# Optimization experiments

Measured on AMD Instinct MI355X. Metric: run time of the kernel, lower is better.

## Reference

```python
import jax, jax.numpy as jnp
import numpy as np

C = 2          # n_channels
F = 32         # n_fields
H = 1024       # hidden_size
B = 16         # batch
S = 2048       # sequence length


def setup_inputs() -> dict:
    key = jax.random.key(0)
    ks = jax.random.split(key, 5)
    hidden = jax.random.normal(ks[0], (B, S, H), dtype=jnp.float32)
    # per-channel learned parameters
    emb = jax.random.normal(ks[1], (C, F, H), dtype=jnp.float32) * 0.02
    scale = 1.0 / np.sqrt(H)
    Wk = jax.random.normal(ks[2], (C, H, H), dtype=jnp.float32) * scale
    Wq = jax.random.normal(ks[3], (C, H, H), dtype=jnp.float32) * scale
    Wv = jax.random.normal(ks[4], (C, H, H), dtype=jnp.float32) * scale
    return {"hidden": hidden, "emb": emb, "Wk": Wk, "Wq": Wq, "Wv": Wv}


def reference(hidden, emb, Wk, Wq, Wv):
    # per-channel linear projections (nn.Linear: x @ W.T), vectorized over channels
    # hidden: [B,S,H], W*: [C,H_out,H_in] -> [C,B,S,H]
    key = jnp.einsum('bsh,coh->cbso', hidden, Wk)
    query = jnp.einsum('bsh,coh->cbso', hidden, Wq)
    value = jnp.einsum('bsh,coh->cbso', hidden, Wv)
    # label embeddings broadcast across batch: [C,F,H] -> [C,B,F,H]
    lab = jnp.broadcast_to(emb[:, None, :, :], (C, hidden.shape[0], F, H))
    # concat label embeddings onto query along token axis: [C,B,S+F,H]
    query = jnp.concatenate([query, lab], axis=2)
    # attention scores (no softmax): [B,C,S+F,S]
    attention = jnp.einsum('cbih,cbjh->bcij', query, key)
    # score[b,c,j,i] = attention[b,c,j,i] * sum_h value[c,b,i,h]
    vsum = jnp.sum(value, axis=-1)          # [C,B,S]
    score = attention * jnp.transpose(vsum, (1, 0, 2))[:, :, None, :]
    return score
```

## Files before the change

kernel.cpp:

```cpp
#include <hip/hip_runtime.h>

typedef unsigned int u32;
typedef unsigned short ushort_t;

typedef __attribute__((ext_vector_type(4))) float f32x4;
typedef __attribute__((ext_vector_type(8))) __bf16 bf16x8;

#define Cc 2
#define Ff 32
#define Hh 1024
#define Bb 16
#define Ss 2048
#define SF 2080

__device__ __forceinline__ ushort_t f2bf(float f) {
  u32 u = __builtin_bit_cast(u32, f);
  u32 r = (u + 0x7fffu + ((u >> 16) & 1u)) >> 16;
  return (ushort_t)r;
}

typedef __attribute__((address_space(1))) const u32 u32_g;
typedef __attribute__((address_space(3))) u32 u32_l;

__device__ __forceinline__ void glds16(const void* g, void* l) {
  __builtin_amdgcn_global_load_lds((u32_g*)g, (u32_l*)l, 16, 0, 0);
}

__device__ __forceinline__ f32x4 mfma16(bf16x8 a, bf16x8 b, f32x4 c) {
  return __builtin_amdgcn_mfma_f32_16x16x32_bf16(a, b, c, 0, 0, 0);
}


__global__ void k_wvsum(const float* __restrict__ Wv, float* __restrict__ wvsum) {
  int idx = blockIdx.y * 256 + threadIdx.x;
  int c = idx >> 10, h = idx & 1023;
  int o0 = blockIdx.x * 128;
  const float* p = Wv + (size_t)c * Hh * Hh + (size_t)o0 * Hh + h;
  float s = 0.f;
#pragma unroll 4
  for (int o = 0; o < 128; ++o) s += p[(size_t)o * Hh];
  atomicAdd(&wvsum[c * Hh + h], s);
}

__global__ void k_hidden(const float* __restrict__ hidden, const float* __restrict__ wvsum,
                         ushort_t* __restrict__ hbf, float* __restrict__ vsum) {
  int row = blockIdx.x;
  int t = threadIdx.x;
  const float4 hv = reinterpret_cast<const float4*>(hidden + (size_t)row * Hh)[t];
  ushort4 o4;
  o4.x = f2bf(hv.x); o4.y = f2bf(hv.y); o4.z = f2bf(hv.z); o4.w = f2bf(hv.w);
  reinterpret_cast<ushort4*>(hbf + (size_t)row * Hh)[t] = o4;
  float4 w0 = reinterpret_cast<const float4*>(wvsum)[t];
  float4 w1 = reinterpret_cast<const float4*>(wvsum + Hh)[t];
  float d0 = hv.x * w0.x + hv.y * w0.y + hv.z * w0.z + hv.w * w0.w;
  float d1 = hv.x * w1.x + hv.y * w1.y + hv.z * w1.z + hv.w * w1.w;
  for (int off = 32; off > 0; off >>= 1) {
    d0 += __shfl_down(d0, off);
    d1 += __shfl_down(d1, off);
  }
  __shared__ float red[2][4];
  int wave = t >> 6, lane = t & 63;
  if (lane == 0) { red[0][wave] = d0; red[1][wave] = d1; }
  __syncthreads();
  if (t == 0) {
    vsum[row]            = red[0][0] + red[0][1] + red[0][2] + red[0][3];
    vsum[Bb * Ss + row]  = red[1][0] + red[1][1] + red[1][2] + red[1][3];
  }
}

__global__ void k_transpose(const float* __restrict__ Wk, const float* __restrict__ Wq,
                            ushort_t* __restrict__ WkT, ushort_t* __restrict__ WqT) {
  __shared__ float t[32][33];
  int zz = blockIdx.z; int mat = zz >> 1, c = zz & 1;
  const float* in = (mat ? Wq : Wk) + (size_t)c * Hh * Hh;
  ushort_t* out = (mat ? WqT : WkT) + (size_t)c * Hh * Hh;
  int h0 = blockIdx.x * 32, o0 = blockIdx.y * 32;
  int tx = threadIdx.x & 31, ty = threadIdx.x >> 5;
#pragma unroll
  for (int i = 0; i < 4; ++i)
    t[ty + 8 * i][tx] = in[(size_t)(o0 + ty + 8 * i) * Hh + h0 + tx];
  __syncthreads();
#pragma unroll
  for (int i = 0; i < 4; ++i)
    out[(size_t)(h0 + ty + 8 * i) * Hh + o0 + tx] = f2bf(t[tx][ty + 8 * i]);
}

__global__ void k_ef(const float* __restrict__ emb, const float* __restrict__ Wk,
                     float* __restrict__ ef) {
  int c = blockIdx.z;
  int h = blockIdx.y * 256 + threadIdx.x;
  int o0 = blockIdx.x * 128;
  __shared__ float es[Ff][129];
  for (int i = threadIdx.x; i < Ff * 128; i += 256) {
    int f = i >> 7, oo = i & 127;
    es[f][oo] = emb[(size_t)(c * Ff + f) * Hh + o0 + oo];
  }
  __syncthreads();
  float acc[Ff];
#pragma unroll
  for (int f = 0; f < Ff; ++f) acc[f] = 0.f;
  for (int oo = 0; oo < 128; ++oo) {
    float wk = Wk[(size_t)c * Hh * Hh + (size_t)(o0 + oo) * Hh + h];
#pragma unroll
    for (int f = 0; f < Ff; ++f) acc[f] += es[f][oo] * wk;
  }
#pragma unroll
  for (int f = 0; f < Ff; ++f)
    atomicAdd(&ef[(size_t)(c * Ff + f) * Hh + h], acc[f]);
}

__global__ void k_ef2g(const float* __restrict__ ef, ushort_t* __restrict__ Gaug) {
  int i = blockIdx.x * 256 + threadIdx.x;
  int c = i >> 15, f = (i >> 10) & 31, h = i & 1023;
  ushort_t v = f2bf(ef[i]);
#pragma unroll
  for (int b = 0; b < Bb; ++b)
    Gaug[((size_t)(c * Bb + b) * SF + Ss + f) * Hh + h] = v;
}

template <int MODE>
__global__ __launch_bounds__(256, 2) void gemm_nt(
    const ushort_t* __restrict__ Aall, const ushort_t* __restrict__ Ball,
    void* __restrict__ Oall, const float* __restrict__ scaleAll) {
  constexpr int BK = 64;
  const int tid = threadIdx.x;
  const int wave = tid >> 6, lane = tid & 63;
  const int wm = wave >> 1, wn = wave & 1;
  const int z = blockIdx.z;
  const int row0 = blockIdx.y * 128;
  const int col0 = blockIdx.x * 128;

  const ushort_t* A; const ushort_t* B;
  if constexpr (MODE == 0) {
    A = Aall + (size_t)z * Hh * Hh;
    B = Ball + (size_t)z * Hh * Hh;
  } else if constexpr (MODE == 1) {
    A = Aall;
    B = Ball + (size_t)z * Hh * Hh;
  } else {
    const int b = z & 15;
    A = Aall + (size_t)z * SF * Hh;
    B = Ball + (size_t)b * Ss * Hh;
  }

  __shared__ ushort_t As[128 * BK];
  __shared__ ushort_t Bs[128 * BK];

  const ushort_t* gA[4]; const ushort_t* gB[4];
  char* lA[4]; char* lB[4];
#pragma unroll
  for (int r = 0; r < 4; ++r) {
    int chunk = r * 256 + wave * 64 + lane;
    int rrow = chunk >> 3, kc = chunk & 7;
    gA[r] = A + (size_t)(row0 + rrow) * Hh + kc * 8;
    gB[r] = B + (size_t)(col0 + rrow) * Hh + kc * 8;
    lA[r] = (char*)As + (r * 256 + wave * 64) * 16;
    lB[r] = (char*)Bs + (r * 256 + wave * 64) * 16;
  }

  f32x4 acc[4][4];
#pragma unroll
  for (int i = 0; i < 4; ++i)
#pragma unroll
    for (int j = 0; j < 4; ++j) acc[i][j] = (f32x4){0.f, 0.f, 0.f, 0.f};

  const int lr = lane & 15, lk = lane >> 4;

  for (int kit = 0; kit < Hh / BK; ++kit) {
#pragma unroll
    for (int r = 0; r < 4; ++r) glds16(gA[r], lA[r]);
#pragma unroll
    for (int r = 0; r < 4; ++r) glds16(gB[r], lB[r]);
#pragma unroll
    for (int r = 0; r < 4; ++r) { gA[r] += BK; gB[r] += BK; }
    __syncthreads();
#pragma unroll
    for (int ks = 0; ks < 2; ++ks) {
      bf16x8 af[4], bfr[4];
#pragma unroll
      for (int mt = 0; mt < 4; ++mt)
        af[mt] = *reinterpret_cast<const bf16x8*>(
            (const char*)As + (wm * 64 + mt * 16 + lr) * 128 + ks * 64 + lk * 16);
#pragma unroll
      for (int nt = 0; nt < 4; ++nt)
        bfr[nt] = *reinterpret_cast<const bf16x8*>(
            (const char*)Bs + (wn * 64 + nt * 16 + lr) * 128 + ks * 64 + lk * 16);
#pragma unroll
      for (int mt = 0; mt < 4; ++mt)
#pragma unroll
        for (int nt = 0; nt < 4; ++nt)
          acc[mt][nt] = mfma16(af[mt], bfr[nt], acc[mt][nt]);
    }
    __syncthreads();
  }

  if constexpr (MODE == 2) {
    const int c = z >> 4, b = z & 15;
    float* Out = (float*)Oall + (size_t)(b * Cc + c) * SF * Ss;
    const float* scale = scaleAll + (size_t)c * (Bb * Ss) + (size_t)b * Ss;
#pragma unroll
    for (int nt = 0; nt < 4; ++nt) {
      int col = col0 + wn * 64 + nt * 16 + lr;
      float s = scale[col];
#pragma unroll
      for (int mt = 0; mt < 4; ++mt) {
        int rbase = row0 + wm * 64 + mt * 16 + lk * 4;
#pragma unroll
        for (int r = 0; r < 4; ++r) {
          int orow = rbase + r;
          if (orow < SF) Out[(size_t)orow * Ss + col] = acc[mt][nt][r] * s;
        }
      }
    }
  } else {
    ushort_t* Out;
    if constexpr (MODE == 0) Out = (ushort_t*)Oall + (size_t)z * Hh * Hh;
    else Out = (ushort_t*)Oall + (size_t)z * (Bb * SF * Hh);
#pragma unroll
    for (int nt = 0; nt < 4; ++nt) {
      int col = col0 + wn * 64 + nt * 16 + lr;
#pragma unroll
      for (int mt = 0; mt < 4; ++mt) {
        int rbase = row0 + wm * 64 + mt * 16 + lk * 4;
#pragma unroll
        for (int r = 0; r < 4; ++r) {
          int m = rbase + r;
          size_t orow;
          if constexpr (MODE == 1) orow = (size_t)(m >> 11) * SF + (m & 2047);
          else orow = (size_t)m;
          Out[orow * Hh + col] = f2bf(acc[mt][nt][r]);
        }
      }
    }
  }
}

extern "C" void kernel_launch(void* const* d_in, const int* in_sizes, int n_in,
                              void* d_out, int out_size, void* d_ws, size_t ws_size,
                              hipStream_t stream) {
  const float* hidden = (const float*)d_in[0];
  const float* emb    = (const float*)d_in[1];
  const float* Wk     = (const float*)d_in[2];
  const float* Wq     = (const float*)d_in[3];
  const float* Wv     = (const float*)d_in[4];
  float* out = (float*)d_out;

  char* base = (char*)d_ws;
  ushort_t* hbf   = (ushort_t*)(base);
  ushort_t* Gaug  = (ushort_t*)(base + 67108864);
  ushort_t* MTb   = (ushort_t*)(base + 203685888);
  ushort_t* WkT   = (ushort_t*)(base + 207880192);
  ushort_t* WqT   = (ushort_t*)(base + 212074496);
  float*    wvsum = (float*)  (base + 216268800);
  float*    efb   = (float*)  (base + 216276992);
  float*    vsum  = (float*)  (base + 216539136);

  hipMemsetAsync(wvsum, 0, 8192 + 262144, stream);

  k_wvsum<<<dim3(8, 8), 256, 0, stream>>>(Wv, wvsum);
  k_hidden<<<Bb * Ss, 256, 0, stream>>>(hidden, wvsum, hbf, vsum);
  k_transpose<<<dim3(32, 32, 4), 256, 0, stream>>>(Wk, Wq, WkT, WqT);
  k_ef<<<dim3(8, 4, 2), 256, 0, stream>>>(emb, Wk, efb);

  gemm_nt<0><<<dim3(8, 8, 2), 256, 0, stream>>>(WkT, WqT, MTb, nullptr);
  gemm_nt<1><<<dim3(8, 256, 2), 256, 0, stream>>>(hbf, MTb, Gaug, nullptr);
  k_ef2g<<<256, 256, 0, stream>>>(efb, Gaug);
  gemm_nt<2><<<dim3(16, 17, 32), 256, 0, stream>>>(Gaug, hbf, out, vsum);
}
```

Measured before the change: 1.324 ms.

## Double-buffer LDS tiles in gemm_nt and swizzle workgroup order across XCDs

Double-buffers the shared-memory A/B tiles so the global-to-LDS load for the next K step is issued before computing the current one. This leaves one barrier per iteration and lets memory latency overlap with MFMA work. It also remaps the flat workgroup id so that consecutive blocks are grouped by (fid mod 8), intended to keep tiles that share data on the same XCD's L2. The cost is doubled LDS use (64KB per block), which may limit occupancy at launch bounds of 2 blocks, and the remap hardcodes grid sizes per mode.

After: 1.477 ms. 11.5% more time.

```diff
diff --git a/kernel.cpp b/kernel.cpp
--- a/kernel.cpp
+++ b/kernel.cpp
@@ -123,12 +123,25 @@
     const ushort_t* __restrict__ Aall, const ushort_t* __restrict__ Ball,
     void* __restrict__ Oall, const float* __restrict__ scaleAll) {
   constexpr int BK = 64;
+  constexpr int NK = Hh / BK;
+  constexpr int GX = (MODE == 0) ? 8 : (MODE == 1) ? 8 : 16;
+  constexpr int GY = (MODE == 0) ? 8 : (MODE == 1) ? 256 : 17;
+  constexpr int GZ = (MODE == 0) ? 2 : (MODE == 1) ? 2 : 32;
+  constexpr int NWG = GX * GY * GZ;
+
   const int tid = threadIdx.x;
   const int wave = tid >> 6, lane = tid & 63;
   const int wm = wave >> 1, wn = wave & 1;
-  const int z = blockIdx.z;
-  const int row0 = blockIdx.y * 128;
-  const int col0 = blockIdx.x * 128;
+
+  int fid = blockIdx.x + GX * (blockIdx.y + GY * blockIdx.z);
+  int swz = (fid & 7) * (NWG >> 3) + (fid >> 3);
+  const int bx = swz % GX;
+  int tt = swz / GX;
+  const int by = tt % GY;
+  const int z  = tt / GY;
+
+  const int row0 = by * 128;
+  const int col0 = bx * 128;
 
   const ushort_t* A; const ushort_t* B;
   if constexpr (MODE == 0) {
@@ -143,8 +156,9 @@
     B = Ball + (size_t)b * Ss * Hh;
   }
 
-  __shared__ ushort_t As[128 * BK];
-  __shared__ ushort_t Bs[128 * BK];
+  __shared__ ushort_t As[2][128 * BK];
+  __shared__ ushort_t Bs[2][128 * BK];
+  constexpr int BUFB = 128 * BK * 2;
 
   const ushort_t* gA[4]; const ushort_t* gB[4];
   char* lA[4]; char* lB[4];
@@ -154,8 +168,8 @@
     int rrow = chunk >> 3, kc = chunk & 7;
     gA[r] = A + (size_t)(row0 + rrow) * Hh + kc * 8;
     gB[r] = B + (size_t)(col0 + rrow) * Hh + kc * 8;
-    lA[r] = (char*)As + (r * 256 + wave * 64) * 16;
-    lB[r] = (char*)Bs + (r * 256 + wave * 64) * 16;
+    lA[r] = (char*)&As[0][0] + (r * 256 + wave * 64) * 16;
+    lB[r] = (char*)&Bs[0][0] + (r * 256 + wave * 64) * 16;
   }
 
   f32x4 acc[4][4];
@@ -166,33 +180,47 @@
 
   const int lr = lane & 15, lk = lane >> 4;
 
-  for (int kit = 0; kit < Hh / BK; ++kit) {
-#pragma unroll
-    for (int r = 0; r < 4; ++r) glds16(gA[r], lA[r]);
-#pragma unroll
-    for (int r = 0; r < 4; ++r) glds16(gB[r], lB[r]);
+  auto stage = [&](int buf) {
+    const int boff = buf * BUFB;
+#pragma unroll
+    for (int r = 0; r < 4; ++r) glds16(gA[r], lA[r] + boff);
+#pragma unroll
+    for (int r = 0; r < 4; ++r) glds16(gB[r], lB[r] + boff);
 #pragma unroll
     for (int r = 0; r < 4; ++r) { gA[r] += BK; gB[r] += BK; }
-    __syncthreads();
+  };
+
+  auto compute = [&](int buf) {
+    const char* asb = (const char*)&As[buf][0];
+    const char* bsb = (const char*)&Bs[buf][0];
 #pragma unroll
     for (int ks = 0; ks < 2; ++ks) {
       bf16x8 af[4], bfr[4];
 #pragma unroll
       for (int mt = 0; mt < 4; ++mt)
         af[mt] = *reinterpret_cast<const bf16x8*>(
-            (const char*)As + (wm * 64 + mt * 16 + lr) * 128 + ks * 64 + lk * 16);
+            asb + (wm * 64 + mt * 16 + lr) * 128 + ks * 64 + lk * 16);
 #pragma unroll
       for (int nt = 0; nt < 4; ++nt)
         bfr[nt] = *reinterpret_cast<const bf16x8*>(
-            (const char*)Bs + (wn * 64 + nt * 16 + lr) * 128 + ks * 64 + lk * 16);
+            bsb + (wn * 64 + nt * 16 + lr) * 128 + ks * 64 + lk * 16);
 #pragma unroll
       for (int mt = 0; mt < 4; ++mt)
 #pragma unroll
         for (int nt = 0; nt < 4; ++nt)
           acc[mt][nt] = mfma16(af[mt], bfr[nt], acc[mt][nt]);
     }
+  };
+
+  stage(0);
+  __syncthreads();
+  for (int kit = 0; kit < NK - 1; ++kit) {
+    const int cur = kit & 1;
+    stage(cur ^ 1);
+    compute(cur);
     __syncthreads();
   }
+  compute((NK - 1) & 1);
 
   if constexpr (MODE == 2) {
     const int c = z >> 4, b = z & 15;
```

## Replace GEMM with 256x256-tile, 512-thread, multi-stage pipelined kernel

Applied to the files above, without the earlier changes.

Replaces the 128x128, single-buffered bf16 MFMA GEMM with 256x256 output tiles computed by 8 waves. Tiles are staged through a ring of LDS slots with BK=32 and loads issued three k-steps ahead, using explicit vmcnt/lgkmcnt waits and a single barrier per step. LDS reads use an XOR swizzle, MFMA sections get raised wave priority, and block IDs are remapped so neighbouring tiles land on the same XCD. The goal is more reuse per tile and global loads hidden behind MFMA work. The cost is 128KB of LDS per block, which limits occupancy, and more wasted rows in the padded final GEMM.

Measured after the change: 1.209 ms. 8.7% less time.

```diff
diff --git a/kernel.cpp b/kernel.cpp
--- a/kernel.cpp
+++ b/kernel.cpp
@@ -119,16 +119,30 @@
 }
 
 template <int MODE>
-__global__ __launch_bounds__(256, 2) void gemm_nt(
+__global__ __launch_bounds__(512, 2) void gemm256(
     const ushort_t* __restrict__ Aall, const ushort_t* __restrict__ Ball,
     void* __restrict__ Oall, const float* __restrict__ scaleAll) {
-  constexpr int BK = 64;
+  constexpr int BK = 32;
+  constexpr int NK = Hh / BK;
+  constexpr int GX = (MODE == 0) ? 4 : (MODE == 1) ? 4 : 8;
+  constexpr int GY = (MODE == 0) ? 4 : (MODE == 1) ? 128 : 9;
+  constexpr int GZ = (MODE == 0) ? 2 : (MODE == 1) ? 2 : 32;
+  constexpr int NWG = GX * GY * GZ;
+
   const int tid = threadIdx.x;
   const int wave = tid >> 6, lane = tid & 63;
-  const int wm = wave >> 1, wn = wave & 1;
-  const int z = blockIdx.z;
-  const int row0 = blockIdx.y * 128;
-  const int col0 = blockIdx.x * 128;
+  const int wm = wave >> 2, wn = wave & 3;
+  const int lr = lane & 15, lk = lane >> 4;
+
+  int fid = blockIdx.x + GX * (blockIdx.y + GY * blockIdx.z);
+  int swz = (fid & 7) * (NWG >> 3) + (fid >> 3);
+  const int bx = swz % GX;
+  int tt2 = swz / GX;
+  const int by = tt2 % GY;
+  const int z  = tt2 / GY;
+
+  const int row0 = by * 256;
+  const int col0 = bx * 256;
 
   const ushort_t* A; const ushort_t* B;
   if constexpr (MODE == 0) {
@@ -143,55 +157,83 @@
     B = Ball + (size_t)b * Ss * Hh;
   }
 
-  __shared__ ushort_t As[128 * BK];
-  __shared__ ushort_t Bs[128 * BK];
-
-  const ushort_t* gA[4]; const ushort_t* gB[4];
-  char* lA[4]; char* lB[4];
-#pragma unroll
-  for (int r = 0; r < 4; ++r) {
-    int chunk = r * 256 + wave * 64 + lane;
-    int rrow = chunk >> 3, kc = chunk & 7;
-    gA[r] = A + (size_t)(row0 + rrow) * Hh + kc * 8;
-    gB[r] = B + (size_t)(col0 + rrow) * Hh + kc * 8;
-    lA[r] = (char*)As + (r * 256 + wave * 64) * 16;
-    lB[r] = (char*)Bs + (r * 256 + wave * 64) * 16;
-  }
-
-  f32x4 acc[4][4];
-#pragma unroll
-  for (int i = 0; i < 4; ++i)
+  __shared__ __align__(16) char lds[131072];
+  char* ldsA = lds;
+  char* ldsB = lds + 65536;
+
+  const int srow = wave * 16 + (lane >> 2);
+  const int kswz = ((lane & 3) ^ ((lane >> 3) & 3)) * 8;
+  const ushort_t* gA0 = A + (size_t)(row0 + srow) * Hh + kswz;
+  const ushort_t* gB0 = B + (size_t)(col0 + srow) * Hh + kswz;
+  const int ldst = wave * 1024;
+
+  auto stgA = [&](int t, int hf) {
+    glds16(gA0 + (size_t)hf * 128 * Hh + t * BK,
+           ldsA + (((2 * t + hf) & 7) << 13) + ldst);
+  };
+  auto stgB = [&](int t, int hf) {
+    glds16(gB0 + (size_t)hf * 128 * Hh + t * BK,
+           ldsB + (((2 * t + hf) & 7) << 13) + ldst);
+  };
+
+  f32x4 acc[8][4];
+#pragma unroll
+  for (int i = 0; i < 8; ++i)
 #pragma unroll
     for (int j = 0; j < 4; ++j) acc[i][j] = (f32x4){0.f, 0.f, 0.f, 0.f};
 
-  const int lr = lane & 15, lk = lane >> 4;
-
-  for (int kit = 0; kit < Hh / BK; ++kit) {
-#pragma unroll
-    for (int r = 0; r < 4; ++r) glds16(gA[r], lA[r]);
-#pragma unroll
-    for (int r = 0; r < 4; ++r) glds16(gB[r], lB[r]);
-#pragma unroll
-    for (int r = 0; r < 4; ++r) { gA[r] += BK; gB[r] += BK; }
-    __syncthreads();
-#pragma unroll
-    for (int ks = 0; ks < 2; ++ks) {
-      bf16x8 af[4], bfr[4];
-#pragma unroll
-      for (int mt = 0; mt < 4; ++mt)
-        af[mt] = *reinterpret_cast<const bf16x8*>(
-            (const char*)As + (wm * 64 + mt * 16 + lr) * 128 + ks * 64 + lk * 16);
+  const int sslot = lk ^ ((lr >> 1) & 3);
+  const int aoff = lr * 64 + sslot * 16;
+  const int boff = ((wn & 1) << 12) + aoff;
+
+#pragma unroll
+  for (int t = 0; t < 3; ++t) {
+    stgA(t, 0); stgA(t, 1); stgB(t, 0); stgB(t, 1);
+  }
+
+  for (int t = 0; t < NK; ++t) {
+    if (t < NK - 2)       asm volatile("s_waitcnt vmcnt(8)" ::: "memory");
+    else if (t == NK - 2) asm volatile("s_waitcnt vmcnt(4)" ::: "memory");
+    else                  asm volatile("s_waitcnt vmcnt(0)" ::: "memory");
+    __builtin_amdgcn_s_barrier();
+    __builtin_amdgcn_sched_barrier(0);
+
+    const char* Apt = ldsA + (((2 * t + wm) & 7) << 13) + aoff;
+    const char* Bpt = ldsB + (((2 * t + (wn >> 1)) & 7) << 13) + boff;
+
+    if (t < NK - 3) { stgA(t + 3, 0); stgA(t + 3, 1); }
+    bf16x8 bfr[4];
+#pragma unroll
+    for (int nt = 0; nt < 4; ++nt)
+      bfr[nt] = *reinterpret_cast<const bf16x8*>(Bpt + nt * 1024);
+    bf16x8 afr[4];
+#pragma unroll
+    for (int mt = 0; mt < 4; ++mt)
+      afr[mt] = *reinterpret_cast<const bf16x8*>(Apt + mt * 1024);
+    asm volatile("s_waitcnt lgkmcnt(0)" ::: "memory");
+    __builtin_amdgcn_sched_barrier(0);
+    __builtin_amdgcn_s_setprio(1);
+#pragma unroll
+    for (int mt = 0; mt < 4; ++mt)
 #pragma unroll
       for (int nt = 0; nt < 4; ++nt)
-        bfr[nt] = *reinterpret_cast<const bf16x8*>(
-            (const char*)Bs + (wn * 64 + nt * 16 + lr) * 128 + ks * 64 + lk * 16);
-#pragma unroll
-      for (int mt = 0; mt < 4; ++mt)
-#pragma unroll
-        for (int nt = 0; nt < 4; ++nt)
-          acc[mt][nt] = mfma16(af[mt], bfr[nt], acc[mt][nt]);
-    }
-    __syncthreads();
+        acc[mt][nt] = mfma16(afr[mt], bfr[nt], acc[mt][nt]);
+    __builtin_amdgcn_s_setprio(0);
+
+    if (t < NK - 3) { stgB(t + 3, 0); stgB(t + 3, 1); }
+    bf16x8 afr2[4];
+#pragma unroll
+    for (int mt = 0; mt < 4; ++mt)
+      afr2[mt] = *reinterpret_cast<const bf16x8*>(Apt + (mt + 4) * 1024);
+    asm volatile("s_waitcnt lgkmcnt(0)" ::: "memory");
+    __builtin_amdgcn_sched_barrier(0);
+    __builtin_amdgcn_s_setprio(1);
+#pragma unroll
+    for (int mt = 0; mt < 4; ++mt)
+#pragma unroll
+      for (int nt = 0; nt < 4; ++nt)
+        acc[mt + 4][nt] = mfma16(afr2[mt], bfr[nt], acc[mt + 4][nt]);
+    __builtin_amdgcn_s_setprio(0);
   }
 
   if constexpr (MODE == 2) {
@@ -203,8 +245,8 @@
       int col = col0 + wn * 64 + nt * 16 + lr;
       float s = scale[col];
 #pragma unroll
-      for (int mt = 0; mt < 4; ++mt) {
-        int rbase = row0 + wm * 64 + mt * 16 + lk * 4;
+      for (int mt = 0; mt < 8; ++mt) {
+        int rbase = row0 + wm * 128 + mt * 16 + lk * 4;
 #pragma unroll
         for (int r = 0; r < 4; ++r) {
           int orow = rbase + r;
@@ -220,8 +262,8 @@
     for (int nt = 0; nt < 4; ++nt) {
       int col = col0 + wn * 64 + nt * 16 + lr;
 #pragma unroll
-      for (int mt = 0; mt < 4; ++mt) {
-        int rbase = row0 + wm * 64 + mt * 16 + lk * 4;
+      for (int mt = 0; mt < 8; ++mt) {
+        int rbase = row0 + wm * 128 + mt * 16 + lk * 4;
 #pragma unroll
         for (int r = 0; r < 4; ++r) {
           int m = rbase + r;
@@ -255,15 +297,15 @@
   float*    efb   = (float*)  (base + 216276992);
   float*    vsum  = (float*)  (base + 216539136);
 
-  hipMemsetAsync(wvsum, 0, 8192 + 262144, stream);
+  (void)hipMemsetAsync(wvsum, 0, 8192 + 262144, stream);
 
   k_wvsum<<<dim3(8, 8), 256, 0, stream>>>(Wv, wvsum);
   k_hidden<<<Bb * Ss, 256, 0, stream>>>(hidden, wvsum, hbf, vsum);
   k_transpose<<<dim3(32, 32, 4), 256, 0, stream>>>(Wk, Wq, WkT, WqT);
   k_ef<<<dim3(8, 4, 2), 256, 0, stream>>>(emb, Wk, efb);
 
-  gemm_nt<0><<<dim3(8, 8, 2), 256, 0, stream>>>(WkT, WqT, MTb, nullptr);
-  gemm_nt<1><<<dim3(8, 256, 2), 256, 0, stream>>>(hbf, MTb, Gaug, nullptr);
+  gemm256<0><<<dim3(4, 4, 2), 512, 0, stream>>>(WkT, WqT, MTb, nullptr);
+  gemm256<1><<<dim3(4, 128, 2), 512, 0, stream>>>(hbf, MTb, Gaug, nullptr);
   k_ef2g<<<256, 256, 0, stream>>>(efb, Gaug);
-  gemm_nt<2><<<dim3(16, 17, 32), 256, 0, stream>>>(Gaug, hbf, out, vsum);
-}
+  gemm256<2><<<dim3(8, 9, 32), 512, 0, stream>>>(Gaug, hbf, out, vsum);
+}
```
